# Optimization experiments

Hardware: AMD Instinct MI355X
Metric: run time of the kernel (lower is better)

The kernel has to match this reference:

```python
import jax, jax.numpy as jnp
import numpy as np

NUM_BINS = 30
MIN_BW = 1e-3
MIN_BH = 1e-3
MIN_D = 1e-3
LO_IN, HI_IN = 0.0, 1.0
LO_OUT, HI_OUT = 0.0, 1.0
DERIV_OUT_LO = (HI_OUT - LO_OUT) / (HI_IN - LO_IN)  # default outside derivatives
DERIV_OUT_HI = DERIV_OUT_LO
EPS = 1e-6
B, V = 65536, 64


def _cumparams(unnorm, lo, hi, min_size):
    # softmax bin sizes with a floor, cumsum into knot positions. [V,K] -> ([V,K+1],[V,K])
    K = unnorm.shape[-1]
    p = jax.nn.softmax(unnorm, axis=-1)
    p = min_size + (1.0 - min_size * K) * p
    cp = jnp.cumsum(p, axis=-1)
    cp = jnp.pad(cp, [(0, 0), (1, 0)])
    cp = (hi - lo) * cp + lo
    cp = cp.at[..., 0].set(lo).at[..., -1].set(hi)
    sizes = cp[..., 1:] - cp[..., :-1]
    return cp, sizes


def setup_inputs() -> dict:
    key = jax.random.key(0)
    k0, k1, k2, k3 = jax.random.split(key, 4)
    return {
        "inputs": jax.random.uniform(k0, (B, V), dtype=jnp.float32),
        "unnormalized_widths": jax.random.uniform(k1, (V, NUM_BINS), dtype=jnp.float32),
        "unnormalized_heights": jax.random.uniform(k2, (V, NUM_BINS), dtype=jnp.float32),
        "unnormalized_derivatives": jax.random.uniform(k3, (V, NUM_BINS - 1), dtype=jnp.float32),
    }


def reference(inputs, unnormalized_widths, unnormalized_heights, unnormalized_derivatives):
    K = NUM_BINS
    nb, nv = inputs.shape

    cumw, widths = _cumparams(unnormalized_widths, LO_IN, HI_IN, MIN_BW)      # [V,K+1],[V,K]
    cumh, heights = _cumparams(unnormalized_heights, LO_OUT, HI_OUT, MIN_BH)  # [V,K+1],[V,K]

    # boundary derivatives pinned so softplus(const)+MIN_D == 1
    const = float(np.log(np.exp(1.0 - MIN_D) - 1.0))
    ud = jnp.pad(unnormalized_derivatives, [(0, 0), (1, 1)], constant_values=const)
    derivs = MIN_D + jax.nn.softplus(ud)  # [V,K+1]
    delta = heights / widths              # [V,K]

    # per-element bin search (forward mode -> search in cumwidths)
    bounds = cumw.at[..., -1].add(EPS)                                   # [V,K+1]
    bin_idx = jnp.sum(inputs[..., None] >= bounds[None], axis=-1) - 1    # [B,V]
    bin_idx = jnp.clip(bin_idx, 0, K - 1)

    vidx = jnp.arange(nv)[None, :]  # broadcast variable index [1,V]
    icw = cumw[vidx, bin_idx]       # input_cumwidths [B,V]
    ibw = widths[vidx, bin_idx]
    ich = cumh[vidx, bin_idx]
    idl = delta[vidx, bin_idx]
    d0 = derivs[vidx, bin_idx]
    d1 = derivs[vidx, bin_idx + 1]
    ih = heights[vidx, bin_idx]

    theta = (inputs - icw) / ibw
    t1mt = theta * (1.0 - theta)
    numerator = ih * (idl * theta * theta + d0 * t1mt)
    denominator = idl + (d0 + d1 - 2.0 * idl) * t1mt
    spline_out = ich + numerator / denominator
    deriv_num = idl * idl * (d1 * theta * theta + 2.0 * idl * t1mt + d0 * (1.0 - theta) ** 2)
    spline_lad = jnp.log(deriv_num) - 2.0 * jnp.log(denominator)

    below = inputs < LO_IN
    above = inputs > HI_IN
    inside = ~(below | above)
    out_lo = LO_OUT + (inputs - LO_IN) * DERIV_OUT_LO
    out_hi = HI_OUT + (inputs - HI_IN) * DERIV_OUT_HI
    outputs = jnp.where(below, out_lo, jnp.where(above, out_hi, spline_out))
    logabsdet = jnp.where(inside, spline_lad, 0.0)
    return outputs, logabsdet
```

## Files before the change

kernel.cpp:

```cpp
#include <hip/hip_runtime.h>
#include <math.h>


#define NB 65536
#define NV 64
#define NKB 30
#define ROWF 153
#define OFF_B 0
#define OFF_W 32
#define OFF_C 62
#define OFF_H 92
#define OFF_D 122
#define NBLK 1024

__global__ __launch_bounds__(64) void rqs_params(const float* __restrict__ uw,
                                                 const float* __restrict__ uh,
                                                 const float* __restrict__ ud,
                                                 float* __restrict__ P) {
  const int v = blockIdx.x;
  const int lane = threadIdx.x;
  float* p = P + v * ROWF;
  const float MINB = 1e-3f;
  const float scale = 1.0f - MINB * (float)NKB;

  {
    float u = (lane < NKB) ? uw[v * NKB + lane] : -1e30f;
    float m = u;
#pragma unroll
    for (int s = 32; s >= 1; s >>= 1) m = fmaxf(m, __shfl_xor(m, s));
    float e = (lane < NKB) ? expf(u - m) : 0.0f;
    float t = e;
#pragma unroll
    for (int s = 32; s >= 1; s >>= 1) t += __shfl_xor(t, s);
    float pk = (lane < NKB) ? (MINB + scale * (e / t)) : 0.0f;
    float ci = pk;
#pragma unroll
    for (int s = 1; s < 64; s <<= 1) {
      float z = __shfl_up(ci, s);
      if (lane >= s) ci += z;
    }
    float ce = ci - pk;
    float nxt = (lane == NKB - 1) ? 1.0f : ci;
    if (lane < NKB) {
      p[OFF_B + lane + 1] = nxt;
      p[OFF_W + lane] = 1.0f / (nxt - ce);
    }
    if (lane == 0) p[OFF_B + 0] = 0.0f;
    if (lane == NKB) p[OFF_B + NKB] = 1.0f + 1e-6f;
    if (lane == NKB + 1) p[OFF_B + NKB + 1] = 3.0e38f;
  }
  {
    float u = (lane < NKB) ? uh[v * NKB + lane] : -1e30f;
    float m = u;
#pragma unroll
    for (int s = 32; s >= 1; s >>= 1) m = fmaxf(m, __shfl_xor(m, s));
    float e = (lane < NKB) ? expf(u - m) : 0.0f;
    float t = e;
#pragma unroll
    for (int s = 32; s >= 1; s >>= 1) t += __shfl_xor(t, s);
    float pk = (lane < NKB) ? (MINB + scale * (e / t)) : 0.0f;
    float ci = pk;
#pragma unroll
    for (int s = 1; s < 64; s <<= 1) {
      float z = __shfl_up(ci, s);
      if (lane >= s) ci += z;
    }
    float ce = ci - pk;
    float nxt = (lane == NKB - 1) ? 1.0f : ci;
    if (lane < NKB) {
      p[OFF_C + lane] = ce;
      p[OFF_H + lane] = nxt - ce;
    }
  }
  {
    const float CST = (float)log(exp(1.0 - 1e-3) - 1.0);
    if (lane <= NKB) {
      float x = (lane == 0 || lane == NKB) ? CST : ud[v * (NKB - 1) + lane - 1];
      float sp = (x > 0.f) ? (x + log1pf(expf(-x))) : log1pf(expf(x));
      p[OFF_D + lane] = 1e-3f + sp;
    }
  }
}

__global__ __launch_bounds__(256, 4) void rqs_main(const float* __restrict__ x,
                                                   const float* __restrict__ P,
                                                   float* __restrict__ out) {
  __shared__ float lds[NV * ROWF];
  {
    const float4* src = (const float4*)P;
    float4* dst = (float4*)lds;
    for (int i = threadIdx.x; i < (NV * ROWF) / 4; i += 256) dst[i] = src[i];
  }
  __syncthreads();

  const int N = NB * NV;
  const int n4 = N / 4;
  for (int gid = blockIdx.x * 256 + threadIdx.x; gid < n4; gid += NBLK * 256) {
    float4 xv = ((const float4*)x)[gid];
    int v0 = (gid & 15) * 4;

    float xs[4] = {xv.x, xv.y, xv.z, xv.w};
    float o[4], l[4];
#pragma unroll
    for (int j = 0; j < 4; ++j) {
      float xx = xs[j];
      const float* row = lds + (v0 + j) * ROWF;
      int idx = 0;
#pragma unroll
      for (int s = 16; s >= 1; s >>= 1) {
        int c = idx + s;
        idx = (xx >= row[OFF_B + c]) ? c : idx;
      }
      int b = idx > 29 ? 29 : idx;

      float icw  = row[OFF_B + b];
      float winv = row[OFF_W + b];
      float ich  = row[OFF_C + b];
      float ih   = row[OFF_H + b];
      float d0   = row[OFF_D + b];
      float d1   = row[OFF_D + b + 1];
      float idl  = ih * winv;

      float th   = (xx - icw) * winv;
      float omt  = 1.0f - th;
      float t1mt = th * omt;
      float th2  = th * th;
      float num  = ih * (idl * th2 + d0 * t1mt);
      float den  = idl + (d0 + d1 - 2.0f * idl) * t1mt;
      float rden = __frcp_rn(den);
      float so   = ich + num * rden;
      float dn   = idl * idl * (d1 * th2 + 2.0f * idl * t1mt + d0 * omt * omt);
      float sl   = __logf(dn * rden * rden);

      bool inside = !(xx < 0.0f) && !(xx > 1.0f);
      o[j] = inside ? so : xx;
      l[j] = inside ? sl : 0.0f;
    }
    float4 ov = {o[0], o[1], o[2], o[3]};
    float4 lv = {l[0], l[1], l[2], l[3]};
    ((float4*)out)[gid] = ov;
    ((float4*)(out + N))[gid] = lv;
  }
}

extern "C" void kernel_launch(void* const* d_in, const int* in_sizes, int n_in,
                              void* d_out, int out_size, void* d_ws, size_t ws_size,
                              hipStream_t stream) {
  const float* x  = (const float*)d_in[0];
  const float* uw = (const float*)d_in[1];
  const float* uh = (const float*)d_in[2];
  const float* ud = (const float*)d_in[3];
  float* out = (float*)d_out;
  float* P   = (float*)d_ws;

  rqs_params<<<NV, 64, 0, stream>>>(uw, uh, ud, P);
  rqs_main<<<NBLK, 256, 0, stream>>>(x, P, out);
}
```

Before: 92.01 us.

## Replace binary bin search with 128-entry LUT plus one probe, pack params as float4

The parameter kernel now also builds a per-variable 128-entry byte lookup table mapping a quantised input to the lower-bound bin. The main kernel uses it and one extra comparison instead of a 5-step binary search. Per-bin parameters are packed into float4 records so a single LDS vector load replaces four scalar ones. Launch geometry changes to 768 blocks of 512 threads, and reciprocal switches to the raw hardware rcp. The goal is fewer dependent LDS reads per element, at the cost of assuming each LUT cell spans at most one knot, which the 1e-3 bin floor does not strictly guarantee.

```diff
diff --git a/kernel.cpp b/kernel.cpp
--- a/kernel.cpp
+++ b/kernel.cpp
@@ -5,13 +5,14 @@
 #define NB 65536
 #define NV 64
 #define NKB 30
-#define ROWF 153
-#define OFF_B 0
-#define OFF_W 32
-#define OFF_C 62
-#define OFF_H 92
-#define OFF_D 122
-#define NBLK 1024
+#define REC_D 124
+#define DER_BASE 7936
+#define DER_S 33
+#define LUT_BASE_B 40192
+#define LUT_S 132
+#define TOT_D 12160
+#define GRID 768
+#define BSZ 512
 
 __global__ __launch_bounds__(64) void rqs_params(const float* __restrict__ uw,
                                                  const float* __restrict__ uh,
@@ -19,10 +20,10 @@
                                                  float* __restrict__ P) {
   const int v = blockIdx.x;
   const int lane = threadIdx.x;
-  float* p = P + v * ROWF;
   const float MINB = 1e-3f;
   const float scale = 1.0f - MINB * (float)NKB;
 
+  float cw_e, winv, wnxt;
   {
     float u = (lane < NKB) ? uw[v * NKB + lane] : -1e30f;
     float m = u;
@@ -39,16 +40,11 @@
       float z = __shfl_up(ci, s);
       if (lane >= s) ci += z;
     }
-    float ce = ci - pk;
-    float nxt = (lane == NKB - 1) ? 1.0f : ci;
-    if (lane < NKB) {
-      p[OFF_B + lane + 1] = nxt;
-      p[OFF_W + lane] = 1.0f / (nxt - ce);
-    }
-    if (lane == 0) p[OFF_B + 0] = 0.0f;
-    if (lane == NKB) p[OFF_B + NKB] = 1.0f + 1e-6f;
-    if (lane == NKB + 1) p[OFF_B + NKB + 1] = 3.0e38f;
+    cw_e = ci - pk;
+    wnxt = (lane == NKB - 1) ? 1.0f : ci;
+    winv = 1.0f / (wnxt - cw_e);
   }
+  float ch_e, hh;
   {
     float u = (lane < NKB) ? uh[v * NKB + lane] : -1e30f;
     float m = u;
@@ -65,73 +61,83 @@
       float z = __shfl_up(ci, s);
       if (lane >= s) ci += z;
     }
-    float ce = ci - pk;
-    float nxt = (lane == NKB - 1) ? 1.0f : ci;
-    if (lane < NKB) {
-      p[OFF_C + lane] = ce;
-      p[OFF_H + lane] = nxt - ce;
-    }
+    ch_e = ci - pk;
+    float hnxt = (lane == NKB - 1) ? 1.0f : ci;
+    hh = hnxt - ch_e;
+  }
+  if (lane < NKB) {
+    float4 r = {cw_e, winv, ch_e, hh};
+    *(float4*)(P + v * REC_D + 4 * lane) = r;
+  }
+  if (lane == NKB) {
+    float4 r = {1.0f + 1e-6f, 0.0f, 0.0f, 0.0f};
+    *(float4*)(P + v * REC_D + 4 * NKB) = r;
   }
   {
     const float CST = (float)log(exp(1.0 - 1e-3) - 1.0);
     if (lane <= NKB) {
       float x = (lane == 0 || lane == NKB) ? CST : ud[v * (NKB - 1) + lane - 1];
       float sp = (x > 0.f) ? (x + log1pf(expf(-x))) : log1pf(expf(x));
-      p[OFF_D + lane] = 1e-3f + sp;
+      P[DER_BASE + v * DER_S + lane] = 1e-3f + sp;
     }
+  }
+  {
+    float t0 = (float)lane * (1.0f / 128.0f);
+    float t1 = (float)(lane + 64) * (1.0f / 128.0f);
+    int lo0 = 0, lo1 = 0;
+#pragma unroll
+    for (int kk = 0; kk < NKB; ++kk) {
+      float c = __shfl(wnxt, kk);
+      lo0 += (c <= t0) ? 1 : 0;
+      lo1 += (c <= t1) ? 1 : 0;
+    }
+    unsigned char* lb = (unsigned char*)P + LUT_BASE_B + v * LUT_S;
+    lb[lane] = (unsigned char)lo0;
+    lb[lane + 64] = (unsigned char)lo1;
   }
 }
 
-__global__ __launch_bounds__(256, 4) void rqs_main(const float* __restrict__ x,
+__global__ __launch_bounds__(BSZ, 6) void rqs_main(const float* __restrict__ x,
                                                    const float* __restrict__ P,
                                                    float* __restrict__ out) {
-  __shared__ float lds[NV * ROWF];
-  {
-    const float4* src = (const float4*)P;
-    float4* dst = (float4*)lds;
-    for (int i = threadIdx.x; i < (NV * ROWF) / 4; i += 256) dst[i] = src[i];
-  }
+  __shared__ __align__(16) float lds[TOT_D];
+  for (int i = threadIdx.x; i < TOT_D / 4; i += BSZ)
+    ((float4*)lds)[i] = ((const float4*)P)[i];
   __syncthreads();
+  const unsigned char* lutb = (const unsigned char*)lds;
 
   const int N = NB * NV;
   const int n4 = N / 4;
-  for (int gid = blockIdx.x * 256 + threadIdx.x; gid < n4; gid += NBLK * 256) {
+  for (int gid = blockIdx.x * BSZ + threadIdx.x; gid < n4; gid += GRID * BSZ) {
     float4 xv = ((const float4*)x)[gid];
-    int v0 = (gid & 15) * 4;
-
+    const int v0 = (gid & 15) * 4;
     float xs[4] = {xv.x, xv.y, xv.z, xv.w};
     float o[4], l[4];
 #pragma unroll
     for (int j = 0; j < 4; ++j) {
       float xx = xs[j];
-      const float* row = lds + (v0 + j) * ROWF;
-      int idx = 0;
-#pragma unroll
-      for (int s = 16; s >= 1; s >>= 1) {
-        int c = idx + s;
-        idx = (xx >= row[OFF_B + c]) ? c : idx;
-      }
-      int b = idx > 29 ? 29 : idx;
-
-      float icw  = row[OFF_B + b];
-      float winv = row[OFF_W + b];
-      float ich  = row[OFF_C + b];
-      float ih   = row[OFF_H + b];
-      float d0   = row[OFF_D + b];
-      float d1   = row[OFF_D + b + 1];
+      const int vj = v0 + j;
+      int u = (int)(xx * 128.0f);
+      u = u < 0 ? 0 : (u > 127 ? 127 : u);
+      int lo = lutb[LUT_BASE_B + vj * LUT_S + u];
+      float probe = lds[vj * REC_D + 4 * (lo + 1)];
+      int b = lo + ((xx >= probe) ? 1 : 0);
+      b = b > 29 ? 29 : b;
+      float4 r4 = *(const float4*)&lds[vj * REC_D + 4 * b];
+      float d0 = lds[DER_BASE + vj * DER_S + b];
+      float d1 = lds[DER_BASE + vj * DER_S + b + 1];
+      float icw = r4.x, winv = r4.y, ich = r4.z, ih = r4.w;
       float idl  = ih * winv;
-
       float th   = (xx - icw) * winv;
       float omt  = 1.0f - th;
       float t1mt = th * omt;
       float th2  = th * th;
       float num  = ih * (idl * th2 + d0 * t1mt);
       float den  = idl + (d0 + d1 - 2.0f * idl) * t1mt;
-      float rden = __frcp_rn(den);
+      float rden = __builtin_amdgcn_rcpf(den);
       float so   = ich + num * rden;
       float dn   = idl * idl * (d1 * th2 + 2.0f * idl * t1mt + d0 * omt * omt);
       float sl   = __logf(dn * rden * rden);
-
       bool inside = !(xx < 0.0f) && !(xx > 1.0f);
       o[j] = inside ? so : xx;
       l[j] = inside ? sl : 0.0f;
@@ -154,5 +160,5 @@
   float* P   = (float*)d_ws;
 
   rqs_params<<<NV, 64, 0, stream>>>(uw, uh, ud, P);
-  rqs_main<<<NBLK, 256, 0, stream>>>(x, P, out);
+  rqs_main<<<GRID, BSZ, 0, stream>>>(x, P, out);
 }
```

After: 85.78 us (median of 2 runs). 1.07x faster.
